# Performance work log

Measured on AMD Instinct MI355X. Metric: run time of the kernel, lower is better.

Reference implementation:

```python
import jax, jax.numpy as jnp
import numpy as np

POS_W = 1.0
ANG_W = 1.0
WID_W = 1.0
N = 1048560  # predictions (divisible by 17)
M = 8388480  # total GT grasps = sum(arange(N) % 17)


def setup_inputs() -> dict:
    key = jax.random.key(0)
    k1, k2 = jax.random.split(key)
    pred = jax.random.normal(k1, (N, 6), dtype=jnp.float32)
    all_targets = jax.random.normal(k2, (M, 6), dtype=jnp.float32)
    # ragged counts in [0, 16]; sum == M exactly
    target_counts = (jnp.arange(N, dtype=jnp.int64) % 17)
    return {"pred": pred, "all_targets": all_targets, "target_counts": target_counts}


def _smooth_l1(x):
    a = jnp.abs(x)
    return jnp.where(a < 1.0, 0.5 * x * x, a - 0.5)


def reference(pred, all_targets, target_counts):
    n = pred.shape[0]
    m = all_targets.shape[0]
    # segment id for each GT row (contiguous slices, order of target_counts)
    seg = jnp.repeat(jnp.arange(n), target_counts, total_repeat_length=m)  # (M,)
    p = pred[seg]  # (M,6) gathered predictions
    dp = p[:, :2] - all_targets[:, :2]
    da = p[:, 2:4] - all_targets[:, 2:4]
    dw = p[:, 4] - all_targets[:, 4]
    dist = (POS_W * jnp.sum(dp * dp, axis=-1)
            + ANG_W * jnp.sum(da * da, axis=-1)
            + WID_W * dw * dw)  # (M,)
    # ragged argmin per segment (first occurrence, like torch.argmin)
    min_d = jax.ops.segment_min(dist, seg, num_segments=n)  # (N,)
    row = jnp.arange(m)
    cand = jnp.where(dist == min_d[seg], row, m)
    arg = jax.ops.segment_min(cand, seg, num_segments=n)  # (N,) global row idx or m
    has = target_counts > 0
    gt = all_targets[jnp.where(has, jnp.clip(arg, 0, m - 1), 0)]  # (N,6)
    # fused per-prediction loss against the closest GT
    loss_pos = jnp.sum(_smooth_l1(pred[:, :2] - gt[:, :2]), axis=-1)
    loss_ang = jnp.sum(jnp.abs(pred[:, 2:4] - gt[:, 2:4]), axis=-1)
    loss_wid = _smooth_l1(pred[:, 4] - gt[:, 4])
    losses = jnp.where(has, POS_W * loss_pos + ANG_W * loss_ang + WID_W * loss_wid, 0.0)
    return jnp.mean(losses)  # reduction='mean'
```

## Files before the change

### kernel.cpp

```cpp
#include <hip/hip_runtime.h>
#include <math.h>
#include <stdint.h>

#define POS_W 1.0f
#define ANG_W 1.0f
#define WID_W 1.0f
#define CHUNK 682
#define SEGS 16
#define SEGS_PER_WAVE 4

__device__ __forceinline__ float smooth_l1(float x) {
    float a = fabsf(x);
    return a < 1.0f ? 0.5f * x * x : a - 0.5f;
}

__device__ __forceinline__ void gl_lds16(const float4* g, float4* l) {
    __builtin_amdgcn_global_load_lds(
        (const __attribute__((address_space(1))) void*)g,
        (__attribute__((address_space(3))) void*)l, 16, 0, 0);
}

__global__ void k_block_sums(const int* __restrict__ counts, int stride, int n,
                             int* __restrict__ blockSums) {
    int i = blockIdx.x * 256 + threadIdx.x;
    int c = (i < n) ? counts[(long long)i * stride] : 0;
    for (int off = 32; off > 0; off >>= 1) c += __shfl_down(c, off, 64);
    __shared__ int sdata[4];
    int lane = threadIdx.x & 63, wave = threadIdx.x >> 6;
    if (lane == 0) sdata[wave] = c;
    __syncthreads();
    if (threadIdx.x == 0)
        blockSums[blockIdx.x] = sdata[0] + sdata[1] + sdata[2] + sdata[3];
}

__global__ __launch_bounds__(256) void k_loss(
    const float* __restrict__ pred, const float* __restrict__ tgt,
    const int* __restrict__ counts, int stride, int n, int mrows,
    const int* __restrict__ blockSums, float invN, float* __restrict__ out) {
    __shared__ float4 bufs[2][SEGS * 64];
    __shared__ int wsum[4];
    __shared__ int wpre[4];
    __shared__ float fs[4];

    int t = threadIdx.x;
    int lane = t & 63, wave = t >> 6;
    int b = blockIdx.x;
    int i = b * 256 + t;
    int c = (i < n) ? counts[(long long)i * stride] : 0;

    int pre = 0;
    for (int j = t; j < b; j += 256) pre += blockSums[j];

    int incl = c;
#pragma unroll
    for (int d = 1; d < 64; d <<= 1) {
        int v = __shfl_up(incl, d, 64);
        if (lane >= d) incl += v;
    }
    for (int o = 32; o > 0; o >>= 1) pre += __shfl_down(pre, o, 64);
    if (lane == 63) wsum[wave] = incl;
    if (lane == 0) wpre[wave] = pre;
    __syncthreads();

    int w0 = wsum[0], w1 = wsum[1], w2 = wsum[2], w3 = wsum[3];
    int waveOff = (wave > 0 ? w0 : 0) + (wave > 1 ? w1 : 0) + (wave > 2 ? w2 : 0);
    int off = waveOff + incl - c;
    int total = w0 + w1 + w2 + w3;
    int winStart = wpre[0] + wpre[1] + wpre[2] + wpre[3];

    bool active = (i < n) && (c > 0);
    float p0 = 0, p1 = 0, p2 = 0, p3 = 0, p4 = 0;
    if (active) {
        const float2* p2p = (const float2*)(pred + (long long)i * 6);
        float2 a = p2p[0], bb = p2p[1], w = p2p[2];
        p0 = a.x; p1 = a.y; p2 = bb.x; p3 = bb.y; p4 = w.x;
    }

    long long winB = (long long)winStart * 24;
    long long alignedB = winB & ~15ll;
    long long base4 = alignedB >> 4;
    int sh = (int)(winStart & 1);
    long long f4last = (((long long)mrows * 24) >> 4) - 1;
    const float4* tgt4 = (const float4*)tgt;

    auto issue_chunk = [&](int bi, int chunkBase) {
        long long q0 = base4 + (((long long)chunkBase * 3) >> 1);
#pragma unroll
        for (int k = 0; k < SEGS_PER_WAVE; ++k) {
            int seg = wave + 4 * k;
            long long gi = q0 + seg * 64 + lane;
            if (gi > f4last) gi = f4last;
            gl_lds16(tgt4 + gi, &bufs[bi][seg * 64]);
        }
    };

    float best = INFINITY;
    float b0 = 0, b1 = 0, b2 = 0, b3 = 0, b4 = 0;

    if (total > 0) issue_chunk(0, 0);

    int cur = 0;
    for (int base = 0; base < total; base += CHUNK, cur ^= 1) {
        int nbase = base + CHUNK;
        if (nbase < total) {
            issue_chunk(cur ^ 1, nbase);
            asm volatile("s_waitcnt vmcnt(4)" ::: "memory");
        } else {
            asm volatile("s_waitcnt vmcnt(0)" ::: "memory");
        }
        __builtin_amdgcn_s_barrier();
        __builtin_amdgcn_sched_barrier(0);

        if (active) {
            int rows = min(CHUNK, total - base);
            const float2* ch2 = (const float2*)&bufs[cur][0];
            int lo = max(off, base), hi = min(off + c, base + rows);
            for (int rr = lo; rr < hi; ++rr) {
                int l2i = (rr - base) * 3 + sh;
                float2 ga = ch2[l2i], gb = ch2[l2i + 1], gw = ch2[l2i + 2];
                float d0 = p0 - ga.x, d1 = p1 - ga.y;
                float d2 = p2 - gb.x, d3 = p3 - gb.y;
                float d4 = p4 - gw.x;
                float dist = POS_W * (d0 * d0 + d1 * d1) +
                             ANG_W * (d2 * d2 + d3 * d3) + WID_W * d4 * d4;
                if (dist < best) {
                    best = dist;
                    b0 = ga.x; b1 = ga.y; b2 = gb.x; b3 = gb.y; b4 = gw.x;
                }
            }
        }
        asm volatile("s_waitcnt lgkmcnt(0)" ::: "memory");
        __builtin_amdgcn_s_barrier();
        __builtin_amdgcn_sched_barrier(0);
    }

    float loss = 0.0f;
    if (active) {
        loss = POS_W * (smooth_l1(p0 - b0) + smooth_l1(p1 - b1)) +
               ANG_W * (fabsf(p2 - b2) + fabsf(p3 - b3)) +
               WID_W * smooth_l1(p4 - b4);
    }

    for (int o = 32; o > 0; o >>= 1) loss += __shfl_down(loss, o, 64);
    if (lane == 0) fs[wave] = loss;
    __syncthreads();
    if (t == 0) {
        float tot = (fs[0] + fs[1] + fs[2] + fs[3]) * invN;
        atomicAdd(out, tot);
    }
}

extern "C" void kernel_launch(void* const* d_in, const int* in_sizes, int n_in,
                              void* d_out, int out_size, void* d_ws,
                              size_t ws_size, hipStream_t stream) {
    const float* pred = (const float*)d_in[0];
    const float* tgt = (const float*)d_in[1];
    const int* counts = (const int*)d_in[2];
    int n = in_sizes[0] / 6;
    int mrows = in_sizes[1] / 6;
    int stride = (in_sizes[2] == n) ? 1 : 2;
    int nb = (n + 255) / 256;

    int* blockSums = (int*)d_ws;
    float* out = (float*)d_out;

    hipMemsetAsync(d_out, 0, sizeof(float), stream);
    k_block_sums<<<nb, 256, 0, stream>>>(counts, stride, n, blockSums);
    k_loss<<<nb, 256, 0, stream>>>(pred, tgt, counts, stride, n, mrows,
                                   blockSums, 1.0f / n, out);
}
```

Baseline: 314.4 us.

## Replace double-buffered chunk loop with single large chunk sized to block window

Swaps the two 682-row LDS buffers for one 2176-row buffer, large enough that a block's whole target window (about 2040 rows with this count pattern) usually loads in one pass. Each wave issues only as many 64-lane segments as the window needs, and the trailing barrier is skipped on the last iteration. The prediction load is also moved ahead of the first __syncthreads so its latency overlaps the scan. This removes per-chunk barriers and wasted tail loads, but drops the overlap between loading the next chunk and computing on the current one, and the larger LDS footprint per block may lower occupancy.

```diff
diff --git a/kernel.cpp b/kernel.cpp
--- a/kernel.cpp
+++ b/kernel.cpp
@@ -5,9 +5,8 @@
 #define POS_W 1.0f
 #define ANG_W 1.0f
 #define WID_W 1.0f
-#define CHUNK 682
-#define SEGS 16
-#define SEGS_PER_WAVE 4
+#define CHUNKR 2176
+#define SEGMAX 52
 
 __device__ __forceinline__ float smooth_l1(float x) {
     float a = fabsf(x);
@@ -37,7 +36,7 @@
     const float* __restrict__ pred, const float* __restrict__ tgt,
     const int* __restrict__ counts, int stride, int n, int mrows,
     const int* __restrict__ blockSums, float invN, float* __restrict__ out) {
-    __shared__ float4 bufs[2][SEGS * 64];
+    __shared__ float4 buf[SEGMAX * 64];
     __shared__ int wsum[4];
     __shared__ int wpre[4];
     __shared__ float fs[4];
@@ -60,6 +59,14 @@
     for (int o = 32; o > 0; o >>= 1) pre += __shfl_down(pre, o, 64);
     if (lane == 63) wsum[wave] = incl;
     if (lane == 0) wpre[wave] = pre;
+
+    bool active = (i < n) && (c > 0);
+    float p0 = 0, p1 = 0, p2 = 0, p3 = 0, p4 = 0;
+    if (active) {
+        const float2* p2p = (const float2*)(pred + (long long)i * 6);
+        float2 a = p2p[0], bb = p2p[1], w = p2p[2];
+        p0 = a.x; p1 = a.y; p2 = bb.x; p3 = bb.y; p4 = w.x;
+    }
     __syncthreads();
 
     int w0 = wsum[0], w1 = wsum[1], w2 = wsum[2], w3 = wsum[3];
@@ -68,52 +75,31 @@
     int total = w0 + w1 + w2 + w3;
     int winStart = wpre[0] + wpre[1] + wpre[2] + wpre[3];
 
-    bool active = (i < n) && (c > 0);
-    float p0 = 0, p1 = 0, p2 = 0, p3 = 0, p4 = 0;
-    if (active) {
-        const float2* p2p = (const float2*)(pred + (long long)i * 6);
-        float2 a = p2p[0], bb = p2p[1], w = p2p[2];
-        p0 = a.x; p1 = a.y; p2 = bb.x; p3 = bb.y; p4 = w.x;
-    }
-
     long long winB = (long long)winStart * 24;
-    long long alignedB = winB & ~15ll;
-    long long base4 = alignedB >> 4;
+    long long base4 = (winB & ~15ll) >> 4;
     int sh = (int)(winStart & 1);
     long long f4last = (((long long)mrows * 24) >> 4) - 1;
     const float4* tgt4 = (const float4*)tgt;
-
-    auto issue_chunk = [&](int bi, int chunkBase) {
-        long long q0 = base4 + (((long long)chunkBase * 3) >> 1);
-#pragma unroll
-        for (int k = 0; k < SEGS_PER_WAVE; ++k) {
-            int seg = wave + 4 * k;
-            long long gi = q0 + seg * 64 + lane;
-            if (gi > f4last) gi = f4last;
-            gl_lds16(tgt4 + gi, &bufs[bi][seg * 64]);
-        }
-    };
+    const float2* ch2 = (const float2*)buf;
 
     float best = INFINITY;
     float b0 = 0, b1 = 0, b2 = 0, b3 = 0, b4 = 0;
 
-    if (total > 0) issue_chunk(0, 0);
-
-    int cur = 0;
-    for (int base = 0; base < total; base += CHUNK, cur ^= 1) {
-        int nbase = base + CHUNK;
-        if (nbase < total) {
-            issue_chunk(cur ^ 1, nbase);
-            asm volatile("s_waitcnt vmcnt(4)" ::: "memory");
-        } else {
-            asm volatile("s_waitcnt vmcnt(0)" ::: "memory");
+    for (int base = 0; base < total; base += CHUNKR) {
+        int rows = min(CHUNKR, total - base);
+        int nF4 = (rows * 3 + sh + 1) >> 1;
+        int nSeg = (nF4 + 63) >> 6;
+        long long q0 = base4 + (((long long)base * 3) >> 1);
+        for (int seg = wave; seg < nSeg; seg += 4) {
+            long long gi = q0 + (long long)(seg << 6) + lane;
+            if (gi > f4last) gi = f4last;
+            gl_lds16(tgt4 + gi, &buf[seg * 64]);
         }
+        asm volatile("s_waitcnt vmcnt(0)" ::: "memory");
         __builtin_amdgcn_s_barrier();
         __builtin_amdgcn_sched_barrier(0);
 
         if (active) {
-            int rows = min(CHUNK, total - base);
-            const float2* ch2 = (const float2*)&bufs[cur][0];
             int lo = max(off, base), hi = min(off + c, base + rows);
             for (int rr = lo; rr < hi; ++rr) {
                 int l2i = (rr - base) * 3 + sh;
@@ -129,9 +115,11 @@
                 }
             }
         }
-        asm volatile("s_waitcnt lgkmcnt(0)" ::: "memory");
-        __builtin_amdgcn_s_barrier();
-        __builtin_amdgcn_sched_barrier(0);
+        if (base + CHUNKR < total) {
+            asm volatile("s_waitcnt lgkmcnt(0)" ::: "memory");
+            __builtin_amdgcn_s_barrier();
+            __builtin_amdgcn_sched_barrier(0);
+        }
     }
 
     float loss = 0.0f;
```

Measured after the change: 303.0 us. 1.04x faster.
